# Kernel tuning notes

Measured on AMD Instinct MI355X. Metric: run time of the kernel, lower is better.

The kernel has to match this reference:

```python
import jax, jax.numpy as jnp
import numpy as np

WS = 8            # window_size
SHIFT = WS // 2   # cyclic shift for 'SW' type
HEAD_DIM = 32

def _rel_index(ws):
    # pairwise relative coordinate indices within a window, offset to [0, 2ws-2]
    cord = np.array([[i, j] for i in range(ws) for j in range(ws)])
    rel = cord[:, None, :] - cord[None, :, :] + ws - 1
    return rel[:, :, 0], rel[:, :, 1]

def _shift_mask(h_w, w_w, p):
    # boolean attention mask for shifted windows; True = masked (-inf)
    s = p - SHIFT
    m = np.zeros((h_w, w_w, p, p, p, p), dtype=bool)
    m[-1, :, :s, :, s:, :] = True
    m[-1, :, s:, :, :s, :] = True
    m[:, -1, :, :s, :, s:] = True
    m[:, -1, :, s:, :, :s] = True
    return m.reshape(h_w * w_w, p * p, p * p)

def setup_inputs() -> dict:
    key = jax.random.key(0)
    ks = jax.random.split(key, 6)
    b, H, W, c = 4, 256, 256, 256
    nh = c // HEAD_DIM
    return {
        "x": jax.random.normal(ks[0], (b, H, W, c), jnp.float32),
        "W_qkv": jax.random.normal(ks[1], (c, 3 * c), jnp.float32) * 0.02,
        "b_qkv": jnp.zeros((3 * c,), jnp.float32),
        "rel_pos": jax.random.normal(ks[2], (nh, 2 * WS - 1, 2 * WS - 1), jnp.float32) * 0.02,
        "W_out": jax.random.normal(ks[3], (c, c), jnp.float32) * 0.02,
        "b_out": jnp.zeros((c,), jnp.float32),
    }

def reference(x, W_qkv, b_qkv, rel_pos, W_out, b_out):
    b, H, W, c = x.shape
    nh = c // HEAD_DIM
    scale = HEAD_DIM ** -0.5
    # cyclic shift (type == 'SW')
    x = jnp.roll(x, (-SHIFT, -SHIFT), axis=(1, 2))
    hw, ww = H // WS, W // WS
    nw, p2 = hw * ww, WS * WS
    # partition into windows: [b, nw, p2, c]
    xw = x.reshape(b, hw, WS, ww, WS, c).transpose(0, 1, 3, 2, 4, 5).reshape(b, nw, p2, c)
    # QKV projection; layout of out dim is (3, n_heads, head_dim)
    qkv = (xw @ W_qkv + b_qkv).reshape(b, nw, p2, 3, nh, HEAD_DIM)
    q, k, v = qkv[..., 0, :, :], qkv[..., 1, :, :], qkv[..., 2, :, :]
    # attention scores per head/window: [h, b, nw, p2, p2]
    sim = jnp.einsum('bwphc,bwqhc->hbwpq', q, k) * scale
    ri, rj = _rel_index(WS)
    sim = sim + rel_pos[:, ri, rj][:, None, None]            # relative position bias
    mask = jnp.asarray(_shift_mask(hw, ww, WS))              # [nw, p2, p2]
    sim = jnp.where(mask[None, None], -jnp.inf, sim)
    probs = jax.nn.softmax(sim, axis=-1)
    out = jnp.einsum('hbwpq,bwqhc->bwphc', probs, v).reshape(b, nw, p2, nh * HEAD_DIM)
    out = out @ W_out + b_out
    # un-window: [b, H, W, c_out]
    out = out.reshape(b, hw, ww, WS, WS, -1).transpose(0, 1, 3, 2, 4, 5).reshape(b, H, W, -1)
    return jnp.roll(out, (SHIFT, SHIFT), axis=(1, 2))
```

## Files before the change

### kernel.cpp

```cpp
#include <hip/hip_runtime.h>
#include <hip/hip_bf16.h>

typedef __attribute__((ext_vector_type(4))) float f32x4;
typedef __attribute__((ext_vector_type(2))) unsigned int u32x2;
typedef __attribute__((ext_vector_type(8))) short s16x8;
typedef __attribute__((ext_vector_type(8))) __bf16 bf16v8;
typedef __attribute__((ext_vector_type(8))) _Float16 f16v8;
typedef __attribute__((ext_vector_type(4))) _Float16 f16x4;

#define LDS_XS 0
#define LDS_QS 32768
#define LDS_KS 65536
#define LDS_VT 98304
#define LDS_TOT 131072

__device__ __forceinline__ f32x4 mfma16(s16x8 a, s16x8 b, f32x4 c) {
  return __builtin_amdgcn_mfma_f32_16x16x32_bf16(
      __builtin_bit_cast(bf16v8, a), __builtin_bit_cast(bf16v8, b), c, 0, 0, 0);
}
__device__ __forceinline__ f32x4 mfma16h(s16x8 a, s16x8 b, f32x4 c) {
  return __builtin_amdgcn_mfma_f32_16x16x32_f16(
      __builtin_bit_cast(f16v8, a), __builtin_bit_cast(f16v8, b), c, 0, 0, 0);
}
__device__ __forceinline__ f32x4 mfmah16(f16x4 a, f16x4 b, f32x4 c) {
  return __builtin_amdgcn_mfma_f32_16x16x16f16(a, b, c, 0, 0, 0);
}

__device__ __forceinline__ unsigned int cvt2(float a, float b) {
  __hip_bfloat162 r = __float22bfloat162_rn(make_float2(a, b));
  unsigned int u;
  __builtin_memcpy(&u, &r, 4);
  return u;
}
__device__ __forceinline__ unsigned int cvt2h(float a, float b) {
  auto r = __builtin_amdgcn_cvt_pkrtz(a, b);
  unsigned int u;
  __builtin_memcpy(&u, &r, 4);
  return u;
}
__device__ __forceinline__ f16x4 pack4h(float a, float b, float c, float d) {
  u32x2 u;
  u.x = cvt2h(a, b);
  u.y = cvt2h(c, d);
  f16x4 r;
  __builtin_memcpy(&r, &u, 8);
  return r;
}

__device__ __forceinline__ short f2bf(float f) {
  unsigned u = __float_as_uint(f);
  u += 0x7fffu + ((u >> 16) & 1u);
  return (short)(u >> 16);
}

__device__ __forceinline__ int swz512(int row, int colByte) {
  return row * 512 + (colByte ^ ((row & 7) << 4));
}
__device__ __forceinline__ int swz128(int row, int colByte) {
  return row * 128 + (colByte ^ ((row & 7) << 4));
}

__global__ void prep_w(const float* __restrict__ Wqkv, const float* __restrict__ Wout,
                       const float* __restrict__ relp,
                       short* __restrict__ wqkvT, short* __restrict__ wH,
                       float* __restrict__ relt) {
  int t = blockIdx.x * 256 + threadIdx.x;
  if (t < 768 * 256) {
    int n = t >> 8, k = t & 255;
    wqkvT[t] = f2bf(Wqkv[k * 768 + n]);
  } else if (t < 768 * 256 + 256 * 256) {
    int t2 = t - 768 * 256;
    int n = t2 >> 8, k = t2 & 255;
    _Float16 h = (_Float16)Wout[k * 256 + n];
    unsigned short us;
    __builtin_memcpy(&us, &h, 2);
    wH[t2] = (short)us;
  } else {
    int u = t - 768 * 256 - 256 * 256;
    int r = u & 3, l = (u >> 2) & 63, strip = (u >> 8) & 3;
    int qt = (u >> 10) & 3, h = (u >> 12) & 7, var = (u >> 15) & 3;
    int p = strip * 16 + (l & 15);
    int q = qt * 16 + ((l >> 4) << 2) + r;
    int pi = p >> 3, pj = p & 7, qi = q >> 3, qj = q & 7;
    bool mrow = (var >> 1) & 1, mcol = var & 1;
    bool mk = (mrow && ((pi < 4) != (qi < 4))) || (mcol && ((pj < 4) != (qj < 4)));
    relt[u] = mk ? -1e30f : relp[h * 225 + (pi - qi + 7) * 15 + (pj - qj + 7)];
  }
}

__global__ __launch_bounds__(512, 2) void swin_mfma(
    const float* __restrict__ x, const float* __restrict__ bqkv,
    const float* __restrict__ bout,
    const short* __restrict__ wqkvT, const short* __restrict__ wH,
    const float* __restrict__ relt, float* __restrict__ out)
{
  __shared__ __align__(16) char lds[LDS_TOT];

  const int tx = threadIdx.x;
  const int w  = tx >> 6;
  const int l  = tx & 63;
  const int g  = l >> 4;
  const int li = l & 15;

  const int b   = blockIdx.x >> 10;
  const int wdw = blockIdx.x & 1023;
  const int wh  = wdw >> 5, wwi = wdw & 31;

  for (int i = 0; i < 8; ++i) {
    int idx = tx + i * 512;
    int p = idx >> 6, c4 = idx & 63;
    int pi = p >> 3, pj = p & 7;
    int sr = (wh * 8 + pi + 4) & 255;
    int sc = (wwi * 8 + pj + 4) & 255;
    f32x4 v = *(const f32x4*)(x + ((((size_t)b * 256 + sr) * 256 + sc) * 256 + c4 * 4));
    u32x2 uu;
    uu.x = cvt2(v[0], v[1]);
    uu.y = cvt2(v[2], v[3]);
    *(u32x2*)(lds + LDS_XS + swz512(p, c4 * 8)) = uu;
  }

  int ocol[6];
  #pragma unroll
  for (int j = 0; j < 4; ++j) ocol[j] = (w * 4 + j) * 16 + li;
  #pragma unroll
  for (int j = 4; j < 6; ++j) ocol[j] = 512 + (w * 2 + (j - 4)) * 16 + li;
  s16x8 bcur[6];
  #pragma unroll
  for (int j = 0; j < 6; ++j)
    bcur[j] = *(const s16x8*)(wqkvT + (size_t)ocol[j] * 256 + g * 8);

  __syncthreads();

  {
    f32x4 acc[6][4];
    #pragma unroll
    for (int j = 0; j < 6; ++j)
      #pragma unroll
      for (int rb = 0; rb < 4; ++rb)
        acc[j][rb] = (f32x4){0.f, 0.f, 0.f, 0.f};

    s16x8 a[2][4];
    #pragma unroll
    for (int rb = 0; rb < 4; ++rb)
      a[0][rb] = *(const s16x8*)(lds + LDS_XS + swz512(rb * 16 + li, g * 16));

    #pragma unroll
    for (int kk = 0; kk < 8; ++kk) {
      const int cur = kk & 1;
      s16x8 bnext[6];
      if (kk < 7) {
        #pragma unroll
        for (int rb = 0; rb < 4; ++rb)
          a[cur ^ 1][rb] = *(const s16x8*)(lds + LDS_XS
                                           + swz512(rb * 16 + li, (kk + 1) * 64 + g * 16));
        #pragma unroll
        for (int j = 0; j < 6; ++j)
          bnext[j] = *(const s16x8*)(wqkvT + (size_t)ocol[j] * 256 + (kk + 1) * 32 + g * 8);
      }
      #pragma unroll
      for (int j = 0; j < 4; ++j)
        #pragma unroll
        for (int rb = 0; rb < 4; ++rb)
          acc[j][rb] = mfma16(bcur[j], a[cur][rb], acc[j][rb]);
      #pragma unroll
      for (int j = 4; j < 6; ++j)
        #pragma unroll
        for (int rb = 0; rb < 4; ++rb)
          acc[j][rb] = mfma16(a[cur][rb], bcur[j], acc[j][rb]);
      if (kk < 7) {
        #pragma unroll
        for (int j = 0; j < 6; ++j) bcur[j] = bnext[j];
      }
    }

    #pragma unroll
    for (int j = 0; j < 4; ++j) {
      const int cb = w * 4 + j;
      if (cb < 16) {
        f32x4 bq = *(const f32x4*)(bqkv + cb * 16 + g * 4);
        #pragma unroll
        for (int rb = 0; rb < 4; ++rb) {
          const float SC = 0.17677669529663687f;
          u32x2 uu;
          uu.x = cvt2((acc[j][rb][0] + bq[0]) * SC, (acc[j][rb][1] + bq[1]) * SC);
          uu.y = cvt2((acc[j][rb][2] + bq[2]) * SC, (acc[j][rb][3] + bq[3]) * SC);
          *(u32x2*)(lds + LDS_QS + swz512(rb * 16 + li, cb * 32 + g * 8)) = uu;
        }
      } else {
        f32x4 bk = *(const f32x4*)(bqkv + cb * 16 + g * 4);
        #pragma unroll
        for (int rb = 0; rb < 4; ++rb) {
          u32x2 uu;
          uu.x = cvt2(acc[j][rb][0] + bk[0], acc[j][rb][1] + bk[1]);
          uu.y = cvt2(acc[j][rb][2] + bk[2], acc[j][rb][3] + bk[3]);
          *(u32x2*)(lds + LDS_KS + swz512(rb * 16 + li, (cb - 16) * 32 + g * 8)) = uu;
        }
      }
    }
    #pragma unroll
    for (int j = 4; j < 6; ++j) {
      const int d = (w * 2 + (j - 4)) * 16 + li;
      const float bv = bqkv[512 + d];
      #pragma unroll
      for (int rb = 0; rb < 4; ++rb) {
        u32x2 uu;
        uu.x = cvt2h(acc[j][rb][0] + bv, acc[j][rb][1] + bv);
        uu.y = cvt2h(acc[j][rb][2] + bv, acc[j][rb][3] + bv);
        *(u32x2*)(lds + LDS_VT + swz128(d, rb * 32 + g * 8)) = uu;
      }
    }
  }
  __syncthreads();

  {
    const int rvar = ((wh == 31) ? 2 : 0) | ((wwi == 31) ? 1 : 0);
    const int phalf = w & 1, p0 = phalf * 32;

    f32x4 rc2[2][2][4];
    s16x8 qf2[2][2], kf2[2][4];
    f16x4 vf2[2][2][4];
    #pragma unroll
    for (int u = 0; u < 2; ++u) {
      const int h = (w >> 1) + u * 4;
      #pragma unroll
      for (int pt = 0; pt < 2; ++pt)
        qf2[u][pt] = *(const s16x8*)(lds + LDS_QS + swz512(p0 + pt * 16 + li, h * 64 + g * 16));
      #pragma unroll
      for (int qt = 0; qt < 4; ++qt)
        kf2[u][qt] = *(const s16x8*)(lds + LDS_KS + swz512(qt * 16 + li, h * 64 + g * 16));
      #pragma unroll
      for (int dt = 0; dt < 2; ++dt)
        #pragma unroll
        for (int qt = 0; qt < 4; ++qt)
          vf2[u][dt][qt] = *(const f16x4*)(lds + LDS_VT
                                           + swz128(h * 32 + dt * 16 + li, qt * 32 + g * 8));
      #pragma unroll
      for (int pt = 0; pt < 2; ++pt)
        #pragma unroll
        for (int qt = 0; qt < 4; ++qt)
          rc2[u][pt][qt] = *(const f32x4*)(relt
              + ((((rvar * 8 + h) * 4 + qt) * 4 + (phalf * 2 + pt)) * 64 + l) * 4);
    }

    #pragma unroll
    for (int u = 0; u < 2; ++u) {
      const int h = (w >> 1) + u * 4;

      f32x4 simT[2][4];
      #pragma unroll
      for (int pt = 0; pt < 2; ++pt)
        #pragma unroll
        for (int qt = 0; qt < 4; ++qt)
          simT[pt][qt] = mfma16(kf2[u][qt], qf2[u][pt], rc2[u][pt][qt]);

      float rinv[2];
      f16x4 pa[2][4];
      #pragma unroll
      for (int pt = 0; pt < 2; ++pt) {
        float s = 0.f;
        #pragma unroll
        for (int qt = 0; qt < 4; ++qt) {
          float e0 = __expf(simT[pt][qt][0]);
          float e1 = __expf(simT[pt][qt][1]);
          float e2 = __expf(simT[pt][qt][2]);
          float e3 = __expf(simT[pt][qt][3]);
          s += (e0 + e1) + (e2 + e3);
          pa[pt][qt] = pack4h(e0, e1, e2, e3);
        }
        s += __shfl_xor(s, 16);
        s += __shfl_xor(s, 32);
        rinv[pt] = 1.0f / s;
      }

      f32x4 at[2][2];
      #pragma unroll
      for (int pt = 0; pt < 2; ++pt)
        #pragma unroll
        for (int dt = 0; dt < 2; ++dt)
          at[pt][dt] = (f32x4){0.f, 0.f, 0.f, 0.f};
      #pragma unroll
      for (int qt = 0; qt < 4; ++qt)
        #pragma unroll
        for (int pt = 0; pt < 2; ++pt)
          #pragma unroll
          for (int dt = 0; dt < 2; ++dt)
            at[pt][dt] = mfmah16(vf2[u][dt][qt], pa[pt][qt], at[pt][dt]);

      #pragma unroll
      for (int pt = 0; pt < 2; ++pt)
        #pragma unroll
        for (int dt = 0; dt < 2; ++dt) {
          const f32x4 a4 = at[pt][dt];
          u32x2 hh;
          hh.x = cvt2h(a4[0] * rinv[pt], a4[1] * rinv[pt]);
          hh.y = cvt2h(a4[2] * rinv[pt], a4[3] * rinv[pt]);
          *(u32x2*)(lds + LDS_XS + swz512(p0 + pt * 16 + li, h * 64 + dt * 32 + g * 8)) = hh;
        }
    }
  }
  __syncthreads();

  {
    f32x4 acc2[2][4];
    #pragma unroll
    for (int c = 0; c < 2; ++c)
      #pragma unroll
      for (int rb = 0; rb < 4; ++rb)
        acc2[c][rb] = (f32x4){0.f, 0.f, 0.f, 0.f};

    s16x8 bc[2];
    #pragma unroll
    for (int c = 0; c < 2; ++c)
      bc[c] = *(const s16x8*)(wH + (size_t)((w * 2 + c) * 16 + li) * 256 + g * 8);

    s16x8 a[2][4];
    #pragma unroll
    for (int rb = 0; rb < 4; ++rb)
      a[0][rb] = *(const s16x8*)(lds + LDS_XS + swz512(rb * 16 + li, g * 16));

    #pragma unroll
    for (int kk = 0; kk < 8; ++kk) {
      const int cur = kk & 1;
      s16x8 bn[2];
      if (kk < 7) {
        #pragma unroll
        for (int rb = 0; rb < 4; ++rb)
          a[cur ^ 1][rb] = *(const s16x8*)(lds + LDS_XS
                                           + swz512(rb * 16 + li, (kk + 1) * 64 + g * 16));
        #pragma unroll
        for (int c = 0; c < 2; ++c)
          bn[c] = *(const s16x8*)(wH + (size_t)((w * 2 + c) * 16 + li) * 256
                                  + (kk + 1) * 32 + g * 8);
      }
      #pragma unroll
      for (int c = 0; c < 2; ++c)
        #pragma unroll
        for (int rb = 0; rb < 4; ++rb)
          acc2[c][rb] = mfma16h(a[cur][rb], bc[c], acc2[c][rb]);
      if (kk < 7) {
        #pragma unroll
        for (int c = 0; c < 2; ++c) bc[c] = bn[c];
      }
    }

    #pragma unroll
    for (int c = 0; c < 2; ++c) {
      const int n = (w * 2 + c) * 16 + li;
      const float bo = bout[n];
      #pragma unroll
      for (int rb = 0; rb < 4; ++rb)
        #pragma unroll
        for (int r = 0; r < 4; ++r) {
          int m = rb * 16 + g * 4 + r;
          int pi = m >> 3, pj = m & 7;
          int dr = (wh * 8 + pi + 4) & 255;
          int dc = (wwi * 8 + pj + 4) & 255;
          out[(((size_t)b * 256 + dr) * 256 + dc) * 256 + n] = acc2[c][rb][r] + bo;
        }
    }
  }
}

extern "C" void kernel_launch(void* const* d_in, const int* in_sizes, int n_in,
                              void* d_out, int out_size, void* d_ws, size_t ws_size,
                              hipStream_t stream) {
  (void)in_sizes; (void)n_in; (void)out_size; (void)ws_size;
  const float* x    = (const float*)d_in[0];
  const float* Wqkv = (const float*)d_in[1];
  const float* bqkv = (const float*)d_in[2];
  const float* relp = (const float*)d_in[3];
  const float* Wout = (const float*)d_in[4];
  const float* bout = (const float*)d_in[5];
  float* out = (float*)d_out;

  short* wqkvT = (short*)d_ws;
  short* wH    = wqkvT + 768 * 256;
  float* relt  = (float*)(wH + 256 * 256);

  hipLaunchKernelGGL(prep_w, dim3(1536), dim3(256), 0, stream,
                     Wqkv, Wout, relp, wqkvT, wH, relt);
  hipLaunchKernelGGL(swin_mfma, dim3(4096), dim3(512), 0, stream,
                     x, bqkv, bout, wqkvT, wH, relt, out);
}
```

Measured before the change: 393.6 us.

## Make swin kernel persistent over 16 windows with prefetch of next window input

```diff
diff --git a/kernel.cpp b/kernel.cpp
--- a/kernel.cpp
+++ b/kernel.cpp
@@ -8,10 +8,8 @@
 typedef __attribute__((ext_vector_type(8))) _Float16 f16v8;
 typedef __attribute__((ext_vector_type(4))) _Float16 f16x4;
 
-#define LDS_XS 0
-#define LDS_QS 32768
-#define LDS_KS 65536
-#define LDS_VT 98304
+#define KS_OFF 65536
+#define VT_OFF 98304
 #define LDS_TOT 131072
 
 __device__ __forceinline__ f32x4 mfma16(s16x8 a, s16x8 b, f32x4 c) {
@@ -102,262 +100,305 @@
   const int g  = l >> 4;
   const int li = l & 15;
 
-  const int b   = blockIdx.x >> 10;
-  const int wdw = blockIdx.x & 1023;
-  const int wh  = wdw >> 5, wwi = wdw & 31;
-
-  for (int i = 0; i < 8; ++i) {
-    int idx = tx + i * 512;
-    int p = idx >> 6, c4 = idx & 63;
-    int pi = p >> 3, pj = p & 7;
-    int sr = (wh * 8 + pi + 4) & 255;
-    int sc = (wwi * 8 + pj + 4) & 255;
-    f32x4 v = *(const f32x4*)(x + ((((size_t)b * 256 + sr) * 256 + sc) * 256 + c4 * 4));
-    u32x2 uu;
-    uu.x = cvt2(v[0], v[1]);
-    uu.y = cvt2(v[2], v[3]);
-    *(u32x2*)(lds + LDS_XS + swz512(p, c4 * 8)) = uu;
-  }
-
   int ocol[6];
   #pragma unroll
   for (int j = 0; j < 4; ++j) ocol[j] = (w * 4 + j) * 16 + li;
   #pragma unroll
   for (int j = 4; j < 6; ++j) ocol[j] = 512 + (w * 2 + (j - 4)) * 16 + li;
-  s16x8 bcur[6];
-  #pragma unroll
-  for (int j = 0; j < 6; ++j)
-    bcur[j] = *(const s16x8*)(wqkvT + (size_t)ocol[j] * 256 + g * 8);
-
-  __syncthreads();
 
   {
-    f32x4 acc[6][4];
-    #pragma unroll
-    for (int j = 0; j < 6; ++j)
-      #pragma unroll
-      for (int rb = 0; rb < 4; ++rb)
-        acc[j][rb] = (f32x4){0.f, 0.f, 0.f, 0.f};
-
-    s16x8 a[2][4];
-    #pragma unroll
-    for (int rb = 0; rb < 4; ++rb)
-      a[0][rb] = *(const s16x8*)(lds + LDS_XS + swz512(rb * 16 + li, g * 16));
-
-    #pragma unroll
-    for (int kk = 0; kk < 8; ++kk) {
-      const int cur = kk & 1;
-      s16x8 bnext[6];
-      if (kk < 7) {
-        #pragma unroll
-        for (int rb = 0; rb < 4; ++rb)
-          a[cur ^ 1][rb] = *(const s16x8*)(lds + LDS_XS
-                                           + swz512(rb * 16 + li, (kk + 1) * 64 + g * 16));
-        #pragma unroll
-        for (int j = 0; j < 6; ++j)
-          bnext[j] = *(const s16x8*)(wqkvT + (size_t)ocol[j] * 256 + (kk + 1) * 32 + g * 8);
-      }
-      #pragma unroll
-      for (int j = 0; j < 4; ++j)
-        #pragma unroll
-        for (int rb = 0; rb < 4; ++rb)
-          acc[j][rb] = mfma16(bcur[j], a[cur][rb], acc[j][rb]);
-      #pragma unroll
-      for (int j = 4; j < 6; ++j)
-        #pragma unroll
-        for (int rb = 0; rb < 4; ++rb)
-          acc[j][rb] = mfma16(a[cur][rb], bcur[j], acc[j][rb]);
-      if (kk < 7) {
-        #pragma unroll
-        for (int j = 0; j < 6; ++j) bcur[j] = bnext[j];
-      }
-    }
-
-    #pragma unroll
-    for (int j = 0; j < 4; ++j) {
-      const int cb = w * 4 + j;
-      if (cb < 16) {
-        f32x4 bq = *(const f32x4*)(bqkv + cb * 16 + g * 4);
-        #pragma unroll
-        for (int rb = 0; rb < 4; ++rb) {
-          const float SC = 0.17677669529663687f;
-          u32x2 uu;
-          uu.x = cvt2((acc[j][rb][0] + bq[0]) * SC, (acc[j][rb][1] + bq[1]) * SC);
-          uu.y = cvt2((acc[j][rb][2] + bq[2]) * SC, (acc[j][rb][3] + bq[3]) * SC);
-          *(u32x2*)(lds + LDS_QS + swz512(rb * 16 + li, cb * 32 + g * 8)) = uu;
-        }
-      } else {
-        f32x4 bk = *(const f32x4*)(bqkv + cb * 16 + g * 4);
-        #pragma unroll
-        for (int rb = 0; rb < 4; ++rb) {
-          u32x2 uu;
-          uu.x = cvt2(acc[j][rb][0] + bk[0], acc[j][rb][1] + bk[1]);
-          uu.y = cvt2(acc[j][rb][2] + bk[2], acc[j][rb][3] + bk[3]);
-          *(u32x2*)(lds + LDS_KS + swz512(rb * 16 + li, (cb - 16) * 32 + g * 8)) = uu;
-        }
-      }
-    }
-    #pragma unroll
-    for (int j = 4; j < 6; ++j) {
-      const int d = (w * 2 + (j - 4)) * 16 + li;
-      const float bv = bqkv[512 + d];
-      #pragma unroll
-      for (int rb = 0; rb < 4; ++rb) {
-        u32x2 uu;
-        uu.x = cvt2h(acc[j][rb][0] + bv, acc[j][rb][1] + bv);
-        uu.y = cvt2h(acc[j][rb][2] + bv, acc[j][rb][3] + bv);
-        *(u32x2*)(lds + LDS_VT + swz128(d, rb * 32 + g * 8)) = uu;
-      }
+    const int win = blockIdx.x * 16;
+    const int b = win >> 10, wdw = win & 1023;
+    const int wh = wdw >> 5, wwi = wdw & 31;
+    for (int i = 0; i < 8; ++i) {
+      int idx = tx + i * 512;
+      int p = idx >> 6, c4 = idx & 63;
+      int pi = p >> 3, pj = p & 7;
+      int sr = (wh * 8 + pi + 4) & 255;
+      int sc = (wwi * 8 + pj + 4) & 255;
+      f32x4 v = *(const f32x4*)(x + ((((size_t)b * 256 + sr) * 256 + sc) * 256 + c4 * 4));
+      u32x2 uu;
+      uu.x = cvt2(v[0], v[1]);
+      uu.y = cvt2(v[2], v[3]);
+      *(u32x2*)(lds + swz512(p, c4 * 8)) = uu;
     }
   }
   __syncthreads();
 
-  {
-    const int rvar = ((wh == 31) ? 2 : 0) | ((wwi == 31) ? 1 : 0);
-    const int phalf = w & 1, p0 = phalf * 32;
-
-    f32x4 rc2[2][2][4];
-    s16x8 qf2[2][2], kf2[2][4];
-    f16x4 vf2[2][2][4];
-    #pragma unroll
-    for (int u = 0; u < 2; ++u) {
-      const int h = (w >> 1) + u * 4;
-      #pragma unroll
-      for (int pt = 0; pt < 2; ++pt)
-        qf2[u][pt] = *(const s16x8*)(lds + LDS_QS + swz512(p0 + pt * 16 + li, h * 64 + g * 16));
-      #pragma unroll
-      for (int qt = 0; qt < 4; ++qt)
-        kf2[u][qt] = *(const s16x8*)(lds + LDS_KS + swz512(qt * 16 + li, h * 64 + g * 16));
-      #pragma unroll
-      for (int dt = 0; dt < 2; ++dt)
+  #pragma unroll 1
+  for (int wi = 0; wi < 16; ++wi) {
+    const int win = blockIdx.x * 16 + wi;
+    const int b   = win >> 10;
+    const int wdw = win & 1023;
+    const int wh  = wdw >> 5, wwi = wdw & 31;
+    const int xr  = (wi & 1) ? 32768 : 0;
+    const int qr  = 32768 - xr;
+
+    {
+      f32x4 acc[6][4];
+      #pragma unroll
+      for (int j = 0; j < 6; ++j)
+        #pragma unroll
+        for (int rb = 0; rb < 4; ++rb)
+          acc[j][rb] = (f32x4){0.f, 0.f, 0.f, 0.f};
+
+      s16x8 bcur[6];
+      #pragma unroll
+      for (int j = 0; j < 6; ++j)
+        bcur[j] = *(const s16x8*)(wqkvT + (size_t)ocol[j] * 256 + g * 8);
+
+      s16x8 a[2][4];
+      #pragma unroll
+      for (int rb = 0; rb < 4; ++rb)
+        a[0][rb] = *(const s16x8*)(lds + xr + swz512(rb * 16 + li, g * 16));
+
+      #pragma unroll
+      for (int kk = 0; kk < 8; ++kk) {
+        const int cur = kk & 1;
+        s16x8 bnext[6];
+        if (kk < 7) {
+          #pragma unroll
+          for (int rb = 0; rb < 4; ++rb)
+            a[cur ^ 1][rb] = *(const s16x8*)(lds + xr
+                                             + swz512(rb * 16 + li, (kk + 1) * 64 + g * 16));
+          #pragma unroll
+          for (int j = 0; j < 6; ++j)
+            bnext[j] = *(const s16x8*)(wqkvT + (size_t)ocol[j] * 256 + (kk + 1) * 32 + g * 8);
+        }
+        #pragma unroll
+        for (int j = 0; j < 4; ++j)
+          #pragma unroll
+          for (int rb = 0; rb < 4; ++rb)
+            acc[j][rb] = mfma16(bcur[j], a[cur][rb], acc[j][rb]);
+        #pragma unroll
+        for (int j = 4; j < 6; ++j)
+          #pragma unroll
+          for (int rb = 0; rb < 4; ++rb)
+            acc[j][rb] = mfma16(a[cur][rb], bcur[j], acc[j][rb]);
+        if (kk < 7) {
+          #pragma unroll
+          for (int j = 0; j < 6; ++j) bcur[j] = bnext[j];
+        }
+      }
+
+      #pragma unroll
+      for (int j = 0; j < 4; ++j) {
+        const int cb = w * 4 + j;
+        if (cb < 16) {
+          f32x4 bq = *(const f32x4*)(bqkv + cb * 16 + g * 4);
+          #pragma unroll
+          for (int rb = 0; rb < 4; ++rb) {
+            const float SC = 0.17677669529663687f;
+            u32x2 uu;
+            uu.x = cvt2((acc[j][rb][0] + bq[0]) * SC, (acc[j][rb][1] + bq[1]) * SC);
+            uu.y = cvt2((acc[j][rb][2] + bq[2]) * SC, (acc[j][rb][3] + bq[3]) * SC);
+            *(u32x2*)(lds + qr + swz512(rb * 16 + li, cb * 32 + g * 8)) = uu;
+          }
+        } else {
+          f32x4 bk = *(const f32x4*)(bqkv + cb * 16 + g * 4);
+          #pragma unroll
+          for (int rb = 0; rb < 4; ++rb) {
+            u32x2 uu;
+            uu.x = cvt2(acc[j][rb][0] + bk[0], acc[j][rb][1] + bk[1]);
+            uu.y = cvt2(acc[j][rb][2] + bk[2], acc[j][rb][3] + bk[3]);
+            *(u32x2*)(lds + KS_OFF + swz512(rb * 16 + li, (cb - 16) * 32 + g * 8)) = uu;
+          }
+        }
+      }
+      #pragma unroll
+      for (int j = 4; j < 6; ++j) {
+        const int d = (w * 2 + (j - 4)) * 16 + li;
+        const float bv = bqkv[512 + d];
+        #pragma unroll
+        for (int rb = 0; rb < 4; ++rb) {
+          u32x2 uu;
+          uu.x = cvt2h(acc[j][rb][0] + bv, acc[j][rb][1] + bv);
+          uu.y = cvt2h(acc[j][rb][2] + bv, acc[j][rb][3] + bv);
+          *(u32x2*)(lds + VT_OFF + swz128(d, rb * 32 + g * 8)) = uu;
+        }
+      }
+    }
+    __syncthreads();
+
+    {
+      const int rvar = ((wh == 31) ? 2 : 0) | ((wwi == 31) ? 1 : 0);
+      const int phalf = w & 1, p0 = phalf * 32;
+
+      f32x4 rc2[2][2][4];
+      s16x8 qf2[2][2], kf2[2][4];
+      f16x4 vf2[2][2][4];
+      #pragma unroll
+      for (int u = 0; u < 2; ++u) {
+        const int h = (w >> 1) + u * 4;
+        #pragma unroll
+        for (int pt = 0; pt < 2; ++pt)
+          qf2[u][pt] = *(const s16x8*)(lds + qr + swz512(p0 + pt * 16 + li, h * 64 + g * 16));
         #pragma unroll
         for (int qt = 0; qt < 4; ++qt)
-          vf2[u][dt][qt] = *(const f16x4*)(lds + LDS_VT
-                                           + swz128(h * 32 + dt * 16 + li, qt * 32 + g * 8));
-      #pragma unroll
-      for (int pt = 0; pt < 2; ++pt)
+          kf2[u][qt] = *(const s16x8*)(lds + KS_OFF + swz512(qt * 16 + li, h * 64 + g * 16));
+        #pragma unroll
+        for (int dt = 0; dt < 2; ++dt)
+          #pragma unroll
+          for (int qt = 0; qt < 4; ++qt)
+            vf2[u][dt][qt] = *(const f16x4*)(lds + VT_OFF
+                                             + swz128(h * 32 + dt * 16 + li, qt * 32 + g * 8));
+        #pragma unroll
+        for (int pt = 0; pt < 2; ++pt)
+          #pragma unroll
+          for (int qt = 0; qt < 4; ++qt)
+            rc2[u][pt][qt] = *(const f32x4*)(relt
+                + ((((rvar * 8 + h) * 4 + qt) * 4 + (phalf * 2 + pt)) * 64 + l) * 4);
+      }
+
+      #pragma unroll
+      for (int u = 0; u < 2; ++u) {
+        const int h = (w >> 1) + u * 4;
+
+        f32x4 simT[2][4];
+        #pragma unroll
+        for (int pt = 0; pt < 2; ++pt)
+          #pragma unroll
+          for (int qt = 0; qt < 4; ++qt)
+            simT[pt][qt] = mfma16(kf2[u][qt], qf2[u][pt], rc2[u][pt][qt]);
+
+        float rinv[2];
+        f16x4 pa[2][4];
+        #pragma unroll
+        for (int pt = 0; pt < 2; ++pt) {
+          float s = 0.f;
+          #pragma unroll
+          for (int qt = 0; qt < 4; ++qt) {
+            float e0 = __expf(simT[pt][qt][0]);
+            float e1 = __expf(simT[pt][qt][1]);
+            float e2 = __expf(simT[pt][qt][2]);
+            float e3 = __expf(simT[pt][qt][3]);
+            s += (e0 + e1) + (e2 + e3);
+            pa[pt][qt] = pack4h(e0, e1, e2, e3);
+          }
+          s += __shfl_xor(s, 16);
+          s += __shfl_xor(s, 32);
+          rinv[pt] = 1.0f / s;
+        }
+
+        f32x4 at[2][2];
+        #pragma unroll
+        for (int pt = 0; pt < 2; ++pt)
+          #pragma unroll
+          for (int dt = 0; dt < 2; ++dt)
+            at[pt][dt] = (f32x4){0.f, 0.f, 0.f, 0.f};
         #pragma unroll
         for (int qt = 0; qt < 4; ++qt)
-          rc2[u][pt][qt] = *(const f32x4*)(relt
-              + ((((rvar * 8 + h) * 4 + qt) * 4 + (phalf * 2 + pt)) * 64 + l) * 4);
+          #pragma unroll
+          for (int pt = 0; pt < 2; ++pt)
+            #pragma unroll
+            for (int dt = 0; dt < 2; ++dt)
+              at[pt][dt] = mfmah16(vf2[u][dt][qt], pa[pt][qt], at[pt][dt]);
+
+        #pragma unroll
+        for (int pt = 0; pt < 2; ++pt)
+          #pragma unroll
+          for (int dt = 0; dt < 2; ++dt) {
+            const f32x4 a4 = at[pt][dt];
+            u32x2 hh;
+            hh.x = cvt2h(a4[0] * rinv[pt], a4[1] * rinv[pt]);
+            hh.y = cvt2h(a4[2] * rinv[pt], a4[3] * rinv[pt]);
+            *(u32x2*)(lds + xr + swz512(p0 + pt * 16 + li, h * 64 + dt * 32 + g * 8)) = hh;
+          }
+      }
     }
-
-    #pragma unroll
-    for (int u = 0; u < 2; ++u) {
-      const int h = (w >> 1) + u * 4;
-
-      f32x4 simT[2][4];
-      #pragma unroll
-      for (int pt = 0; pt < 2; ++pt)
-        #pragma unroll
-        for (int qt = 0; qt < 4; ++qt)
-          simT[pt][qt] = mfma16(kf2[u][qt], qf2[u][pt], rc2[u][pt][qt]);
-
-      float rinv[2];
-      f16x4 pa[2][4];
-      #pragma unroll
-      for (int pt = 0; pt < 2; ++pt) {
-        float s = 0.f;
-        #pragma unroll
-        for (int qt = 0; qt < 4; ++qt) {
-          float e0 = __expf(simT[pt][qt][0]);
-          float e1 = __expf(simT[pt][qt][1]);
-          float e2 = __expf(simT[pt][qt][2]);
-          float e3 = __expf(simT[pt][qt][3]);
-          s += (e0 + e1) + (e2 + e3);
-          pa[pt][qt] = pack4h(e0, e1, e2, e3);
-        }
-        s += __shfl_xor(s, 16);
-        s += __shfl_xor(s, 32);
-        rinv[pt] = 1.0f / s;
-      }
-
-      f32x4 at[2][2];
-      #pragma unroll
-      for (int pt = 0; pt < 2; ++pt)
-        #pragma unroll
-        for (int dt = 0; dt < 2; ++dt)
-          at[pt][dt] = (f32x4){0.f, 0.f, 0.f, 0.f};
-      #pragma unroll
-      for (int qt = 0; qt < 4; ++qt)
-        #pragma unroll
-        for (int pt = 0; pt < 2; ++pt)
-          #pragma unroll
-          for (int dt = 0; dt < 2; ++dt)
-            at[pt][dt] = mfmah16(vf2[u][dt][qt], pa[pt][qt], at[pt][dt]);
-
-      #pragma unroll
-      for (int pt = 0; pt < 2; ++pt)
-        #pragma unroll
-        for (int dt = 0; dt < 2; ++dt) {
-          const f32x4 a4 = at[pt][dt];
-          u32x2 hh;
-          hh.x = cvt2h(a4[0] * rinv[pt], a4[1] * rinv[pt]);
-          hh.y = cvt2h(a4[2] * rinv[pt], a4[3] * rinv[pt]);
-          *(u32x2*)(lds + LDS_XS + swz512(p0 + pt * 16 + li, h * 64 + dt * 32 + g * 8)) = hh;
-        }
+    __syncthreads();
+
+    {
+      const bool has_next = (wi < 15);
+      f32x4 xv[8];
+      if (has_next) {
+        const int nwin = win + 1;
+        const int nb = nwin >> 10, nwdw = nwin & 1023;
+        const int nwh = nwdw >> 5, nwwi = nwdw & 31;
+        #pragma unroll
+        for (int i = 0; i < 8; ++i) {
+          int idx = tx + i * 512;
+          int p = idx >> 6, c4 = idx & 63;
+          int pi = p >> 3, pj = p & 7;
+          int sr = (nwh * 8 + pi + 4) & 255;
+          int sc = (nwwi * 8 + pj + 4) & 255;
+          xv[i] = *(const f32x4*)(x + ((((size_t)nb * 256 + sr) * 256 + sc) * 256 + c4 * 4));
+        }
+        #pragma unroll
+        for (int i = 0; i < 8; ++i) asm volatile("" : "+v"(xv[i]));
+      }
+
+      f32x4 acc2[2][4];
+      #pragma unroll
+      for (int c = 0; c < 2; ++c)
+        #pragma unroll
+        for (int rb = 0; rb < 4; ++rb)
+          acc2[c][rb] = (f32x4){0.f, 0.f, 0.f, 0.f};
+
+      s16x8 bc[2];
+      #pragma unroll
+      for (int c = 0; c < 2; ++c)
+        bc[c] = *(const s16x8*)(wH + (size_t)((w * 2 + c) * 16 + li) * 256 + g * 8);
+
+      s16x8 a[2][4];
+      #pragma unroll
+      for (int rb = 0; rb < 4; ++rb)
+        a[0][rb] = *(const s16x8*)(lds + xr + swz512(rb * 16 + li, g * 16));
+
+      #pragma unroll
+      for (int kk = 0; kk < 8; ++kk) {
+        const int cur = kk & 1;
+        s16x8 bn[2];
+        if (kk < 7) {
+          #pragma unroll
+          for (int rb = 0; rb < 4; ++rb)
+            a[cur ^ 1][rb] = *(const s16x8*)(lds + xr
+                                             + swz512(rb * 16 + li, (kk + 1) * 64 + g * 16));
+          #pragma unroll
+          for (int c = 0; c < 2; ++c)
+            bn[c] = *(const s16x8*)(wH + (size_t)((w * 2 + c) * 16 + li) * 256
+                                    + (kk + 1) * 32 + g * 8);
+        }
+        #pragma unroll
+        for (int c = 0; c < 2; ++c)
+          #pragma unroll
+          for (int rb = 0; rb < 4; ++rb)
+            acc2[c][rb] = mfma16h(a[cur][rb], bc[c], acc2[c][rb]);
+        if (kk < 7) {
+          #pragma unroll
+          for (int c = 0; c < 2; ++c) bc[c] = bn[c];
+        }
+      }
+
+      if (has_next) {
+        #pragma unroll
+        for (int i = 0; i < 8; ++i) {
+          int idx = tx + i * 512;
+          int p = idx >> 6, c4 = idx & 63;
+          u32x2 uu;
+          uu.x = cvt2(xv[i][0], xv[i][1]);
+          uu.y = cvt2(xv[i][2], xv[i][3]);
+          *(u32x2*)(lds + qr + swz512(p, c4 * 8)) = uu;
+        }
+      }
+
+      #pragma unroll
+      for (int c = 0; c < 2; ++c) {
+        const int n = (w * 2 + c) * 16 + li;
+        const float bo = bout[n];
+        #pragma unroll
+        for (int rb = 0; rb < 4; ++rb)
+          #pragma unroll
+          for (int r = 0; r < 4; ++r) {
+            int m = rb * 16 + g * 4 + r;
+            int pi = m >> 3, pj = m & 7;
+            int dr = (wh * 8 + pi + 4) & 255;
+            int dc = (wwi * 8 + pj + 4) & 255;
+            out[(((size_t)b * 256 + dr) * 256 + dc) * 256 + n] = acc2[c][rb][r] + bo;
+          }
+      }
     }
-  }
-  __syncthreads();
-
-  {
-    f32x4 acc2[2][4];
-    #pragma unroll
-    for (int c = 0; c < 2; ++c)
-      #pragma unroll
-      for (int rb = 0; rb < 4; ++rb)
-        acc2[c][rb] = (f32x4){0.f, 0.f, 0.f, 0.f};
-
-    s16x8 bc[2];
-    #pragma unroll
-    for (int c = 0; c < 2; ++c)
-      bc[c] = *(const s16x8*)(wH + (size_t)((w * 2 + c) * 16 + li) * 256 + g * 8);
-
-    s16x8 a[2][4];
-    #pragma unroll
-    for (int rb = 0; rb < 4; ++rb)
-      a[0][rb] = *(const s16x8*)(lds + LDS_XS + swz512(rb * 16 + li, g * 16));
-
-    #pragma unroll
-    for (int kk = 0; kk < 8; ++kk) {
-      const int cur = kk & 1;
-      s16x8 bn[2];
-      if (kk < 7) {
-        #pragma unroll
-        for (int rb = 0; rb < 4; ++rb)
-          a[cur ^ 1][rb] = *(const s16x8*)(lds + LDS_XS
-                                           + swz512(rb * 16 + li, (kk + 1) * 64 + g * 16));
-        #pragma unroll
-        for (int c = 0; c < 2; ++c)
-          bn[c] = *(const s16x8*)(wH + (size_t)((w * 2 + c) * 16 + li) * 256
-                                  + (kk + 1) * 32 + g * 8);
-      }
-      #pragma unroll
-      for (int c = 0; c < 2; ++c)
-        #pragma unroll
-        for (int rb = 0; rb < 4; ++rb)
-          acc2[c][rb] = mfma16h(a[cur][rb], bc[c], acc2[c][rb]);
-      if (kk < 7) {
-        #pragma unroll
-        for (int c = 0; c < 2; ++c) bc[c] = bn[c];
-      }
-    }
-
-    #pragma unroll
-    for (int c = 0; c < 2; ++c) {
-      const int n = (w * 2 + c) * 16 + li;
-      const float bo = bout[n];
-      #pragma unroll
-      for (int rb = 0; rb < 4; ++rb)
-        #pragma unroll
-        for (int r = 0; r < 4; ++r) {
-          int m = rb * 16 + g * 4 + r;
-          int pi = m >> 3, pj = m & 7;
-          int dr = (wh * 8 + pi + 4) & 255;
-          int dc = (wwi * 8 + pj + 4) & 255;
-          out[(((size_t)b * 256 + dr) * 256 + dc) * 256 + n] = acc2[c][rb][r] + bo;
-        }
-    }
+    __syncthreads();
   }
 }
 
@@ -379,6 +420,6 @@
 
   hipLaunchKernelGGL(prep_w, dim3(1536), dim3(256), 0, stream,
                      Wqkv, Wout, relp, wqkvT, wH, relt);
-  hipLaunchKernelGGL(swin_mfma, dim3(4096), dim3(512), 0, stream,
+  hipLaunchKernelGGL(swin_mfma, dim3(256), dim3(512), 0, stream,
                      x, bqkv, bout, wqkvT, wH, relt, out);
 }
```

Measured after the change: 648.2 us. +64.7%, slower.
